# Performance work log

Hardware: AMD Instinct MI355X
Metric: run time of the kernel (lower is better)

Reference implementation:

```python
import jax, jax.numpy as jnp
import numpy as np

B, S, IN, OUT = 4, 2048, 4096, 4096

def setup_inputs() -> dict:
    key = jax.random.key(0)
    k1, k2, k3, k4 = jax.random.split(key, 4)
    input = jax.random.normal(k1, (B, S, IN), dtype=jnp.float32)
    # int8-valued weights stored as int32 (range [-128, 127])
    weight_int8 = jax.random.randint(k2, (OUT, IN), -128, 128, dtype=jnp.int32)
    scale = jax.random.uniform(k3, (OUT, 1), dtype=jnp.float32, minval=0.001, maxval=0.02)
    zero_point = jnp.zeros((OUT, 1), dtype=jnp.float32)
    bias = jax.random.normal(k4, (OUT,), dtype=jnp.float32)
    return {"input": input, "weight_int8": weight_int8, "scale": scale,
            "zero_point": zero_point, "bias": bias}

def reference(input, weight_int8, scale, zero_point, bias):
    # Dequantize: per-output-channel affine (w - zp) * s, then linear.
    w = (weight_int8.astype(input.dtype) - zero_point) * scale  # [OUT, IN]
    out = jnp.einsum('bsi,oi->bso', input, w)
    return out + bias
```

## Files before the change

kernel.cpp:

```cpp
#include <hip/hip_runtime.h>
#include <cstdint>
#include <cstddef>


#define BM 256
#define BN 256
#define BK 32
#define KDIM 4096
#define NT (KDIM / BK)

typedef __bf16 bf16x8 __attribute__((ext_vector_type(8)));
typedef float floatx4 __attribute__((ext_vector_type(4)));
typedef float float4v __attribute__((ext_vector_type(4)));
typedef int int4v __attribute__((ext_vector_type(4)));
typedef unsigned short ushort8v __attribute__((ext_vector_type(8)));

#define AS1 __attribute__((address_space(1)))
#define AS3 __attribute__((address_space(3)))

__device__ __forceinline__ void load16_g2l(const void* g, void* l) {
    __builtin_amdgcn_global_load_lds((const AS1 void*)(uintptr_t)g,
                                     (AS3 void*)(uint32_t)(uintptr_t)l,
                                     16, 0, 0);
}

__device__ __forceinline__ unsigned short f2bf(float f) {
    union { float f; uint32_t u; } v; v.f = f;
    uint32_t u = v.u;
    uint32_t r = (u + 0x7fffu + ((u >> 16) & 1u)) >> 16;
    return (unsigned short)r;
}

__global__ __launch_bounds__(256) void prep(
    const float* __restrict__ a_in, unsigned short* __restrict__ a_out,
    const int* __restrict__ w, const float* __restrict__ scale,
    const float* __restrict__ zp, unsigned short* __restrict__ w_out,
    int ga_units) {
    const long long u = (long long)blockIdx.x * 256 + threadIdx.x;
    if (u < ga_units) {
        const size_t i = (size_t)u * 8;
        float4v f0 = *(const float4v*)(a_in + i);
        float4v f1 = *(const float4v*)(a_in + i + 4);
        ushort8v r;
        r[0] = f2bf(f0[0]); r[1] = f2bf(f0[1]);
        r[2] = f2bf(f0[2]); r[3] = f2bf(f0[3]);
        r[4] = f2bf(f1[0]); r[5] = f2bf(f1[1]);
        r[6] = f2bf(f1[2]); r[7] = f2bf(f1[3]);
        *(ushort8v*)(a_out + i) = r;
    } else {
        const size_t i = (size_t)(u - ga_units) * 8;
        const int row = (int)(i >> 12);
        const float s = scale[row];
        const float z = zp[row];
        int4v w0 = *(const int4v*)(w + i);
        int4v w1 = *(const int4v*)(w + i + 4);
        ushort8v o;
        o[0] = f2bf(((float)w0[0] - z) * s);
        o[1] = f2bf(((float)w0[1] - z) * s);
        o[2] = f2bf(((float)w0[2] - z) * s);
        o[3] = f2bf(((float)w0[3] - z) * s);
        o[4] = f2bf(((float)w1[0] - z) * s);
        o[5] = f2bf(((float)w1[1] - z) * s);
        o[6] = f2bf(((float)w1[2] - z) * s);
        o[7] = f2bf(((float)w1[3] - z) * s);
        *(ushort8v*)(w_out + i) = o;
    }
}

__global__ __launch_bounds__(512, 2) void gemm_bf16_bt(
    const unsigned short* __restrict__ A,
    const unsigned short* __restrict__ Bm,
    const float* __restrict__ bias,
    float* __restrict__ C,
    int M, int N, int K) {
    __shared__ unsigned short lds_a[4][BM * BK];
    __shared__ unsigned short lds_b[4][BN * BK];

    const int tid = threadIdx.x;
    const int lane = tid & 63;
    const int wv = tid >> 6;
    const int wm = (wv >> 2) * 128;
    const int wn = (wv & 3) * 64;

    const int nwg = gridDim.x;
    const int b = blockIdx.x;
    const int swz = (b & 7) * (nwg >> 3) + (b >> 3);
    const int bx = swz & 15;
    const int by = swz >> 4;
    const int n0 = bx * BN;
    const int m0 = by * BM;

    floatx4 acc[8][4];
    const floatx4 zero = {0.f, 0.f, 0.f, 0.f};
#pragma unroll
    for (int i = 0; i < 8; ++i)
#pragma unroll
        for (int j = 0; j < 4; ++j) acc[i][j] = zero;

    const int fl0 = tid, fl1 = tid + 512;
    const int r0 = fl0 >> 2, r1 = fl1 >> 2;
    const int kc0 = ((fl0 & 3) ^ ((r0 >> 1) & 3)) * 8;
    const int kc1 = ((fl1 & 3) ^ ((r1 >> 1) & 3)) * 8;
    const unsigned short* gA0 = A + (size_t)(m0 + r0) * K + kc0;
    const unsigned short* gA1 = A + (size_t)(m0 + r1) * K + kc1;
    const unsigned short* gB0 = Bm + (size_t)(n0 + r0) * K + kc0;
    const unsigned short* gB1 = Bm + (size_t)(n0 + r1) * K + kc1;
    const int lo0 = fl0 * 8, lo1 = fl1 * 8;

    const int fm = lane & 15;
    const int fq = lane >> 4;
    const int swzf = fq ^ ((fm >> 1) & 3);
    int pA[8], pB[4];
#pragma unroll
    for (int i = 0; i < 8; ++i) pA[i] = ((wm + i * 16 + fm) * 4 + swzf) * 8;
#pragma unroll
    for (int j = 0; j < 4; ++j) pB[j] = ((wn + j * 16 + fm) * 4 + swzf) * 8;

#pragma unroll
    for (int tt = 0; tt < 3; ++tt) {
        const int kk = tt * BK;
        unsigned short* sa = lds_a[tt];
        unsigned short* sb = lds_b[tt];
        load16_g2l(gA0 + kk, sa + lo0);
        load16_g2l(gA1 + kk, sa + lo1);
        load16_g2l(gB0 + kk, sb + lo0);
        load16_g2l(gB1 + kk, sb + lo1);
    }
    asm volatile("s_waitcnt vmcnt(8)" ::: "memory");
    __builtin_amdgcn_s_barrier();
    asm volatile("" ::: "memory");

#pragma unroll 1
    for (int t = 0; t < NT; ++t) {
        const unsigned short* la = lds_a[t & 3];
        const unsigned short* lb = lds_b[t & 3];
        const bool st = (t < NT - 3);
        const int kk = (t + 3) * BK;
        unsigned short* sa = lds_a[(t + 3) & 3];
        unsigned short* sb = lds_b[(t + 3) & 3];

        bf16x8 av[4], bv[4];
#pragma unroll
        for (int j = 0; j < 4; ++j) bv[j] = *(const bf16x8*)(lb + pB[j]);
#pragma unroll
        for (int i = 0; i < 4; ++i) av[i] = *(const bf16x8*)(la + pA[i]);
        if (st) {
            load16_g2l(gA0 + kk, sa + lo0);
            load16_g2l(gA1 + kk, sa + lo1);
        }
        __builtin_amdgcn_s_barrier();
        asm volatile("s_waitcnt lgkmcnt(0)" ::: "memory");
        __builtin_amdgcn_s_setprio(1);
#pragma unroll
        for (int i = 0; i < 4; ++i)
#pragma unroll
            for (int j = 0; j < 4; ++j)
                acc[i][j] = __builtin_amdgcn_mfma_f32_16x16x32_bf16(
                    av[i], bv[j], acc[i][j], 0, 0, 0);
        __builtin_amdgcn_s_setprio(0);
        __builtin_amdgcn_s_barrier();

        bf16x8 av2[4];
#pragma unroll
        for (int i = 0; i < 4; ++i) av2[i] = *(const bf16x8*)(la + pA[i + 4]);
        if (st) {
            load16_g2l(gB0 + kk, sb + lo0);
            load16_g2l(gB1 + kk, sb + lo1);
        }
        __builtin_amdgcn_s_barrier();
        asm volatile("s_waitcnt lgkmcnt(0)" ::: "memory");
        __builtin_amdgcn_s_setprio(1);
#pragma unroll
        for (int i = 0; i < 4; ++i)
#pragma unroll
            for (int j = 0; j < 4; ++j)
                acc[i + 4][j] = __builtin_amdgcn_mfma_f32_16x16x32_bf16(
                    av2[i], bv[j], acc[i + 4][j], 0, 0, 0);
        __builtin_amdgcn_s_setprio(0);

        if (t < NT - 3)
            asm volatile("s_waitcnt vmcnt(8)" ::: "memory");
        else if (t == NT - 3)
            asm volatile("s_waitcnt vmcnt(4)" ::: "memory");
        else if (t == NT - 2)
            asm volatile("s_waitcnt vmcnt(0)" ::: "memory");
        __builtin_amdgcn_s_barrier();
        asm volatile("" ::: "memory");
    }

#pragma unroll
    for (int j = 0; j < 4; ++j) {
        const int col = n0 + wn + j * 16 + fm;
        const float bvl = bias[col];
#pragma unroll
        for (int i = 0; i < 8; ++i) {
            const int rbase = m0 + wm + i * 16 + fq * 4;
#pragma unroll
            for (int r = 0; r < 4; ++r) {
                C[(size_t)(rbase + r) * N + col] = acc[i][j][r] + bvl;
            }
        }
    }
}

__global__ __launch_bounds__(256) void fallback_naive(
    const float* __restrict__ in, const int* __restrict__ w,
    const float* __restrict__ scale, const float* __restrict__ zp,
    const float* __restrict__ bias, float* __restrict__ out,
    int M, int N, int K) {
    int idx = blockIdx.x * 256 + threadIdx.x;
    if (idx >= M * N) return;
    int m = idx / N, n = idx - m * N;
    const float s = scale[n], z = zp[n];
    const float* a = in + (size_t)m * K;
    const int* wr = w + (size_t)n * K;
    float acc = 0.f;
    for (int k = 0; k < K; ++k) acc += a[k] * ((float)wr[k] - z);
    out[idx] = acc * s + bias[n];
}

extern "C" void kernel_launch(void* const* d_in, const int* in_sizes, int n_in,
                              void* d_out, int out_size, void* d_ws, size_t ws_size,
                              hipStream_t stream) {
    constexpr int M = 4 * 2048;
    constexpr int K = 4096;
    constexpr int N = 4096;

    const float* input = (const float*)d_in[0];
    const int* w8 = (const int*)d_in[1];
    const float* scale = (const float*)d_in[2];
    const float* zp = (const float*)d_in[3];
    const float* bias = (const float*)d_in[4];
    float* out = (float*)d_out;

    const size_t need = ((size_t)M * K + (size_t)N * K) * sizeof(unsigned short);
    if (ws_size < need) {
        const int total = M * N;
        fallback_naive<<<(total + 255) / 256, 256, 0, stream>>>(
            input, w8, scale, zp, bias, out, M, N, K);
        return;
    }

    unsigned short* wsA = (unsigned short*)d_ws;
    unsigned short* wsW = wsA + (size_t)M * K;

    const int ga_units = (M * K) / 8;
    const int gw_units = (N * K) / 8;
    const int prep_blocks = (ga_units + gw_units) / 256;
    prep<<<prep_blocks, 256, 0, stream>>>(
        input, wsA, w8, scale, zp, wsW, ga_units);

    dim3 grid((N / BN) * (M / BM));
    gemm_bf16_bt<<<grid, 512, 0, stream>>>(wsA, wsW, bias, out, M, N, K);
}
```

Before: 527.1 us.

## Restructure GEMM main loop to BK=64 with half-tile staged quadrant schedule

Doubles the K tile to 64 and replaces the 4-deep ring buffer with a double buffer split into 128-row halves for A and B. Each iteration is broken into four MFMA quadrant phases, and each phase issues the global-to-LDS load for one half of the next tile. This aims to halve the barrier and loop overhead per unit of K and to spread memory traffic evenly across the compute phases. The trade-off is a shallower prefetch distance, plus a new XOR swizzle over 8 chunks whose bank-conflict behaviour changes.

```diff
diff --git a/kernel.cpp b/kernel.cpp
--- a/kernel.cpp
+++ b/kernel.cpp
@@ -5,9 +5,9 @@
 
 #define BM 256
 #define BN 256
-#define BK 32
+#define BK 64
 #define KDIM 4096
-#define NT (KDIM / BK)
+#define NT2 (KDIM / BK)
 
 typedef __bf16 bf16x8 __attribute__((ext_vector_type(8)));
 typedef float floatx4 __attribute__((ext_vector_type(4)));
@@ -73,14 +73,16 @@
     const float* __restrict__ bias,
     float* __restrict__ C,
     int M, int N, int K) {
-    __shared__ unsigned short lds_a[4][BM * BK];
-    __shared__ unsigned short lds_b[4][BN * BK];
+    __shared__ unsigned short lds_a[2][2][8192];
+    __shared__ unsigned short lds_b[2][2][8192];
 
     const int tid = threadIdx.x;
     const int lane = tid & 63;
     const int wv = tid >> 6;
     const int wm = (wv >> 2) * 128;
     const int wn = (wv & 3) * 64;
+    const int ha = wv >> 2;
+    const int hb = (wv & 3) >> 1;
 
     const int nwg = gridDim.x;
     const int b = blockIdx.x;
@@ -97,92 +99,136 @@
 #pragma unroll
         for (int j = 0; j < 4; ++j) acc[i][j] = zero;
 
-    const int fl0 = tid, fl1 = tid + 512;
-    const int r0 = fl0 >> 2, r1 = fl1 >> 2;
-    const int kc0 = ((fl0 & 3) ^ ((r0 >> 1) & 3)) * 8;
-    const int kc1 = ((fl1 & 3) ^ ((r1 >> 1) & 3)) * 8;
-    const unsigned short* gA0 = A + (size_t)(m0 + r0) * K + kc0;
-    const unsigned short* gA1 = A + (size_t)(m0 + r1) * K + kc1;
-    const unsigned short* gB0 = Bm + (size_t)(n0 + r0) * K + kc0;
-    const unsigned short* gB1 = Bm + (size_t)(n0 + r1) * K + kc1;
-    const int lo0 = fl0 * 8, lo1 = fl1 * 8;
+    const int r0 = tid >> 3;
+    const int cofs = (((tid & 7) ^ (r0 & 7)) * 8);
+    const unsigned short* pAs = A + (size_t)(m0 + r0) * K + cofs;
+    const unsigned short* pBs = Bm + (size_t)(n0 + r0) * K + cofs;
+
+    auto stageA = [&](int tile, int half) {
+        const unsigned short* src =
+            pAs + (size_t)half * 128 * K + (size_t)tile * BK;
+        unsigned short* dst = &lds_a[tile & 1][half][tid * 8];
+        load16_g2l(src, dst);
+        load16_g2l(src + (size_t)64 * K, dst + 4096);
+    };
+    auto stageB = [&](int tile, int half) {
+        const unsigned short* src =
+            pBs + (size_t)half * 128 * K + (size_t)tile * BK;
+        unsigned short* dst = &lds_b[tile & 1][half][tid * 8];
+        load16_g2l(src, dst);
+        load16_g2l(src + (size_t)64 * K, dst + 4096);
+    };
 
     const int fm = lane & 15;
     const int fq = lane >> 4;
-    const int swzf = fq ^ ((fm >> 1) & 3);
-    int pA[8], pB[4];
-#pragma unroll
-    for (int i = 0; i < 8; ++i) pA[i] = ((wm + i * 16 + fm) * 4 + swzf) * 8;
-#pragma unroll
-    for (int j = 0; j < 4; ++j) pB[j] = ((wn + j * 16 + fm) * 4 + swzf) * 8;
-
-#pragma unroll
-    for (int tt = 0; tt < 3; ++tt) {
-        const int kk = tt * BK;
-        unsigned short* sa = lds_a[tt];
-        unsigned short* sb = lds_b[tt];
-        load16_g2l(gA0 + kk, sa + lo0);
-        load16_g2l(gA1 + kk, sa + lo1);
-        load16_g2l(gB0 + kk, sb + lo0);
-        load16_g2l(gB1 + kk, sb + lo1);
-    }
-    asm volatile("s_waitcnt vmcnt(8)" ::: "memory");
+    const int kx0 = ((fq) ^ (fm & 7)) * 8;
+    const int kx1 = ((4 + fq) ^ (fm & 7)) * 8;
+    const int rbB = (wn & 64) + fm;
+
+    stageA(0, 0); stageA(0, 1); stageB(0, 0); stageB(0, 1);
+    stageA(1, 0);
+    asm volatile("s_waitcnt vmcnt(2)" ::: "memory");
     __builtin_amdgcn_s_barrier();
     asm volatile("" ::: "memory");
 
 #pragma unroll 1
-    for (int t = 0; t < NT; ++t) {
-        const unsigned short* la = lds_a[t & 3];
-        const unsigned short* lb = lds_b[t & 3];
-        const bool st = (t < NT - 3);
-        const int kk = (t + 3) * BK;
-        unsigned short* sa = lds_a[(t + 3) & 3];
-        unsigned short* sb = lds_b[(t + 3) & 3];
-
-        bf16x8 av[4], bv[4];
-#pragma unroll
-        for (int j = 0; j < 4; ++j) bv[j] = *(const bf16x8*)(lb + pB[j]);
-#pragma unroll
-        for (int i = 0; i < 4; ++i) av[i] = *(const bf16x8*)(la + pA[i]);
-        if (st) {
-            load16_g2l(gA0 + kk, sa + lo0);
-            load16_g2l(gA1 + kk, sa + lo1);
-        }
+    for (int t = 0; t < NT2; ++t) {
+        const int cur = t & 1;
+        const unsigned short* pa = &lds_a[cur][ha][fm * 64];
+        const unsigned short* pb = &lds_b[cur][hb][rbB * 64];
+
+        bf16x8 aLO[4][2], bLO[2][2];
+#pragma unroll
+        for (int i = 0; i < 4; ++i) {
+            aLO[i][0] = *(const bf16x8*)(pa + i * 1024 + kx0);
+            aLO[i][1] = *(const bf16x8*)(pa + i * 1024 + kx1);
+        }
+#pragma unroll
+        for (int j = 0; j < 2; ++j) {
+            bLO[j][0] = *(const bf16x8*)(pb + j * 1024 + kx0);
+            bLO[j][1] = *(const bf16x8*)(pb + j * 1024 + kx1);
+        }
+        if (t + 1 < NT2) stageA(t + 1, 1);
+        asm volatile("" ::: "memory");
         __builtin_amdgcn_s_barrier();
         asm volatile("s_waitcnt lgkmcnt(0)" ::: "memory");
         __builtin_amdgcn_s_setprio(1);
 #pragma unroll
-        for (int i = 0; i < 4; ++i)
-#pragma unroll
-            for (int j = 0; j < 4; ++j)
-                acc[i][j] = __builtin_amdgcn_mfma_f32_16x16x32_bf16(
-                    av[i], bv[j], acc[i][j], 0, 0, 0);
+        for (int s = 0; s < 2; ++s)
+#pragma unroll
+            for (int i = 0; i < 4; ++i)
+#pragma unroll
+                for (int j = 0; j < 2; ++j)
+                    acc[i][j] = __builtin_amdgcn_mfma_f32_16x16x32_bf16(
+                        aLO[i][s], bLO[j][s], acc[i][j], 0, 0, 0);
         __builtin_amdgcn_s_setprio(0);
-        __builtin_amdgcn_s_barrier();
-
-        bf16x8 av2[4];
-#pragma unroll
-        for (int i = 0; i < 4; ++i) av2[i] = *(const bf16x8*)(la + pA[i + 4]);
-        if (st) {
-            load16_g2l(gB0 + kk, sb + lo0);
-            load16_g2l(gB1 + kk, sb + lo1);
-        }
+        asm volatile("" ::: "memory");
+        __builtin_amdgcn_s_barrier();
+        asm volatile("" ::: "memory");
+
+        bf16x8 bHI[2][2];
+#pragma unroll
+        for (int j = 0; j < 2; ++j) {
+            bHI[j][0] = *(const bf16x8*)(pb + (j + 2) * 1024 + kx0);
+            bHI[j][1] = *(const bf16x8*)(pb + (j + 2) * 1024 + kx1);
+        }
+        if (t + 1 < NT2) stageB(t + 1, 0);
+        asm volatile("" ::: "memory");
         __builtin_amdgcn_s_barrier();
         asm volatile("s_waitcnt lgkmcnt(0)" ::: "memory");
         __builtin_amdgcn_s_setprio(1);
 #pragma unroll
-        for (int i = 0; i < 4; ++i)
-#pragma unroll
-            for (int j = 0; j < 4; ++j)
-                acc[i + 4][j] = __builtin_amdgcn_mfma_f32_16x16x32_bf16(
-                    av2[i], bv[j], acc[i + 4][j], 0, 0, 0);
+        for (int s = 0; s < 2; ++s)
+#pragma unroll
+            for (int i = 0; i < 4; ++i)
+#pragma unroll
+                for (int j = 0; j < 2; ++j)
+                    acc[i][j + 2] = __builtin_amdgcn_mfma_f32_16x16x32_bf16(
+                        aLO[i][s], bHI[j][s], acc[i][j + 2], 0, 0, 0);
         __builtin_amdgcn_s_setprio(0);
-
-        if (t < NT - 3)
-            asm volatile("s_waitcnt vmcnt(8)" ::: "memory");
-        else if (t == NT - 3)
-            asm volatile("s_waitcnt vmcnt(4)" ::: "memory");
-        else if (t == NT - 2)
+        asm volatile("" ::: "memory");
+        __builtin_amdgcn_s_barrier();
+        asm volatile("" ::: "memory");
+
+        bf16x8 aHI[4][2];
+#pragma unroll
+        for (int i = 0; i < 4; ++i) {
+            aHI[i][0] = *(const bf16x8*)(pa + (i + 4) * 1024 + kx0);
+            aHI[i][1] = *(const bf16x8*)(pa + (i + 4) * 1024 + kx1);
+        }
+        if (t + 1 < NT2) stageB(t + 1, 1);
+        asm volatile("" ::: "memory");
+        __builtin_amdgcn_s_barrier();
+        asm volatile("s_waitcnt lgkmcnt(0)" ::: "memory");
+        __builtin_amdgcn_s_setprio(1);
+#pragma unroll
+        for (int s = 0; s < 2; ++s)
+#pragma unroll
+            for (int i = 0; i < 4; ++i)
+#pragma unroll
+                for (int j = 0; j < 2; ++j)
+                    acc[i + 4][j + 2] = __builtin_amdgcn_mfma_f32_16x16x32_bf16(
+                        aHI[i][s], bHI[j][s], acc[i + 4][j + 2], 0, 0, 0);
+        __builtin_amdgcn_s_setprio(0);
+        asm volatile("" ::: "memory");
+        __builtin_amdgcn_s_barrier();
+        asm volatile("" ::: "memory");
+
+        if (t + 2 < NT2) stageA(t + 2, 0);
+        __builtin_amdgcn_s_setprio(1);
+#pragma unroll
+        for (int s = 0; s < 2; ++s)
+#pragma unroll
+            for (int i = 0; i < 4; ++i)
+#pragma unroll
+                for (int j = 0; j < 2; ++j)
+                    acc[i + 4][j] = __builtin_amdgcn_mfma_f32_16x16x32_bf16(
+                        aHI[i][s], bLO[j][s], acc[i + 4][j], 0, 0, 0);
+        __builtin_amdgcn_s_setprio(0);
+
+        if (t < NT2 - 2)
+            asm volatile("s_waitcnt vmcnt(2)" ::: "memory");
+        else if (t == NT2 - 2)
             asm volatile("s_waitcnt vmcnt(0)" ::: "memory");
         __builtin_amdgcn_s_barrier();
         asm volatile("" ::: "memory");
```

After: 504.7 us. -4.2%, faster.
